# Performance work log

Hardware: AMD Instinct MI355X
Metric: run time of the kernel (lower is better)

Reference implementation:

```python
import jax, jax.numpy as jnp
import numpy as np
from jax import lax

B, C, O, N, L = 32, 32, 32, 512, 128
K, DIL = 2, 2
PAD = (K - 1) * DIL
EPS = 1e-5


def setup_inputs() -> dict:
    key = jax.random.key(0)
    ks = jax.random.split(key, 14)
    x = jax.random.normal(ks[0], (B, C, N, L), dtype=jnp.float32)
    support0 = jax.random.uniform(ks[1], (N, N), dtype=jnp.float32) / N
    support1 = jax.random.uniform(ks[2], (N, N), dtype=jnp.float32) / N
    filt_w = jax.random.normal(ks[3], (O, C, K), dtype=jnp.float32) * 0.1
    filt_b = jnp.zeros((O,), jnp.float32)
    gate_w = jax.random.normal(ks[4], (O, C, K), dtype=jnp.float32) * 0.1
    gate_b = jnp.zeros((O,), jnp.float32)
    gc_w0 = jax.random.normal(ks[5], (O, O), dtype=jnp.float32) * 0.05  # Linear weight (out,in)
    gc_w1 = jax.random.normal(ks[6], (O, O), dtype=jnp.float32) * 0.05
    gc_b = jnp.zeros((O,), jnp.float32)
    skip_w = jax.random.normal(ks[7], (O, O), dtype=jnp.float32) * 0.05  # 1x1 conv
    skip_b = jnp.zeros((O,), jnp.float32)
    res_w = jax.random.normal(ks[8], (C, O), dtype=jnp.float32) * 0.05   # 1x1 conv
    res_b = jnp.zeros((C,), jnp.float32)
    bn_gamma = jnp.ones((C,), jnp.float32)
    bn_beta = jnp.zeros((C,), jnp.float32)
    return dict(x=x, support0=support0, support1=support1,
                filt_w=filt_w, filt_b=filt_b, gate_w=gate_w, gate_b=gate_b,
                gc_w0=gc_w0, gc_w1=gc_w1, gc_b=gc_b,
                skip_w=skip_w, skip_b=skip_b, res_w=res_w, res_b=res_b,
                bn_gamma=bn_gamma, bn_beta=bn_beta)


def _causal_conv(z, w, b):
    # z: (BN, Cin, L), w: (Cout, Cin, K) -> (BN, Cout, L); left-pad for causality
    y = lax.conv_general_dilated(z, w, window_strides=(1,), padding=[(PAD, 0)],
                                 rhs_dilation=(DIL,),
                                 dimension_numbers=('NCH', 'OIH', 'NCH'))
    return y + b[None, :, None]


def reference(x, support0, support1, filt_w, filt_b, gate_w, gate_b,
              gc_w0, gc_w1, gc_b, skip_w, skip_b, res_w, res_b,
              bn_gamma, bn_beta):
    # x: (B, C, N, L)
    x_flat = x.transpose(0, 2, 1, 3).reshape(B * N, C, L)
    h = jnp.tanh(_causal_conv(x_flat, filt_w, filt_b)) * \
        jax.nn.sigmoid(_causal_conv(x_flat, gate_w, gate_b))  # (B*N, O, L)
    h = h.reshape(B, N, O, L)
    # graph conv fused over all timesteps: supports mix node dim, Linear mixes channel dim
    g0 = jnp.einsum('nm,bmcl->bncl', support0, h)
    g1 = jnp.einsum('nm,bmcl->bncl', support1, h)
    hg = (jnp.einsum('bncl,oc->bnol', g0, gc_w0)
          + jnp.einsum('bncl,oc->bnol', g1, gc_w1)
          + gc_b[None, None, :, None])  # (B, N, O, L)
    skip = jnp.einsum('bncl,oc->bnol', hg, skip_w) + skip_b[None, None, :, None]
    skip = skip.transpose(0, 2, 1, 3)  # (B, O, N, L)
    res = jnp.einsum('bncl,oc->bnol', hg, res_w) + res_b[None, None, :, None]  # (B, N, C, L)
    # BatchNorm1d (training mode: batch statistics over (B*N, L) per channel)
    mean = res.mean(axis=(0, 1, 3))
    var = res.var(axis=(0, 1, 3))
    res_bn = bn_gamma[None, None, :, None] * (res - mean[None, None, :, None]) \
             * lax.rsqrt(var[None, None, :, None] + EPS) + bn_beta[None, None, :, None]
    residual = x + res_bn.transpose(0, 2, 1, 3)  # (B, C, N, L); dropout = identity (eval)
    return residual, skip
```

## Files before the change

kernel.cpp:

```cpp
#include <hip/hip_runtime.h>
#include <cstdint>


typedef unsigned short ushort_t;
typedef unsigned int uint_t;

__device__ __forceinline__ float bf2f(uint_t u) {
  return __uint_as_float(u << 16);
}
__device__ __forceinline__ ushort_t f2bf(float f) {
  uint_t u = __float_as_uint(f);
  u += 0x7fffu + ((u >> 16) & 1u);
  return (ushort_t)(u >> 16);
}

__global__ __launch_bounds__(256) void k0(
    const float* __restrict__ gc_w0, const float* __restrict__ gc_w1,
    const float* __restrict__ gc_b, const float* __restrict__ skip_w,
    const float* __restrict__ skip_b, const float* __restrict__ res_w,
    const float* __restrict__ res_b, float* __restrict__ Wc) {
  const int t = threadIdx.x;
  for (int e = t; e < 4096; e += 256) {
    const int mat = e >> 10, idx = e & 1023, o = idx >> 5, ci = idx & 31;
    const float* left = (mat < 2) ? skip_w : res_w;
    const float* g = (mat & 1) ? gc_w1 : gc_w0;
    float s = 0.f;
    #pragma unroll
    for (int c = 0; c < 32; ++c) s = fmaf(left[o * 32 + c], g[c * 32 + ci], s);
    Wc[mat * 1024 + idx] = s;
  }
  if (t < 32) {
    float s = 0.f, r = 0.f;
    #pragma unroll
    for (int c = 0; c < 32; ++c) {
      s = fmaf(skip_w[t * 32 + c], gc_b[c], s);
      r = fmaf(res_w[t * 32 + c], gc_b[c], r);
    }
    Wc[4096 + t] = s + skip_b[t];
    Wc[4128 + t] = r + res_b[t];
  }
}

__global__ __launch_bounds__(256) void k0b(const float* __restrict__ S0,
                                           const float* __restrict__ S1,
                                           ushort_t* __restrict__ S0b,
                                           ushort_t* __restrict__ S1b) {
  const int i = (blockIdx.x * 256 + threadIdx.x) * 4;
  const float4 a = *(const float4*)(S0 + i);
  const float4 c = *(const float4*)(S1 + i);
  ushort4 pa = make_ushort4(f2bf(a.x), f2bf(a.y), f2bf(a.z), f2bf(a.w));
  ushort4 pc = make_ushort4(f2bf(c.x), f2bf(c.y), f2bf(c.z), f2bf(c.w));
  *(ushort4*)(S0b + i) = pa;
  *(ushort4*)(S1b + i) = pc;
}

__global__ __launch_bounds__(256) void k1a(const float* __restrict__ x,
                                           ushort_t* __restrict__ xT) {
  __shared__ float tile[128 * 65];
  const int nt = blockIdx.x, c = blockIdx.y, b = blockIdx.z;
  const int n0 = nt * 64, t = threadIdx.x;
  const int lq = t & 31, r = t >> 5;
  const float* src = x + (((size_t)(b * 32 + c)) * 512 + n0) * 128;
  for (int nr = 0; nr < 8; ++nr) {
    const int nn = nr * 8 + r;
    const float4 v = *(const float4*)(src + nn * 128 + lq * 4);
    tile[(lq * 4 + 0) * 65 + nn] = v.x;
    tile[(lq * 4 + 1) * 65 + nn] = v.y;
    tile[(lq * 4 + 2) * 65 + nn] = v.z;
    tile[(lq * 4 + 3) * 65 + nn] = v.w;
  }
  __syncthreads();
  const int nn2 = t & 63, lg = t >> 6;
  ushort_t* dst = xT + (size_t)b * 128 * 16384 + (size_t)c * 512 + n0 + nn2;
  for (int i = 0; i < 32; ++i) {
    const int l = lg * 32 + i;
    dst[(size_t)l * 16384] = f2bf(tile[l * 65 + nn2]);
  }
}

__global__ __launch_bounds__(256) void k1(
    const ushort_t* __restrict__ xT, const float* __restrict__ fw,
    const float* __restrict__ fb, const float* __restrict__ gw,
    const float* __restrict__ gb, ushort_t* __restrict__ hA) {
  const int l = blockIdx.x, b = blockIdx.y;
  const int t = threadIdx.x;
  const size_t plane = (size_t)(b * 128 + l) * 16384;
  const size_t planem2 = (size_t)(b * 128 + l - 2) * 16384;
  for (int half = 0; half < 2; ++half) {
    const int n = t + half * 256;
    float x0v[32], xmv[32];
    #pragma unroll
    for (int c = 0; c < 32; ++c) {
      x0v[c] = bf2f(xT[plane + c * 512 + n]);
      xmv[c] = (l >= 2) ? bf2f(xT[planem2 + c * 512 + n]) : 0.f;
    }
    #pragma unroll 4
    for (int o = 0; o < 32; ++o) {
      float f = fb[o], g = gb[o];
      #pragma unroll
      for (int c = 0; c < 32; ++c) {
        const float w0 = fw[(o * 32 + c) * 2], w1 = fw[(o * 32 + c) * 2 + 1];
        f = fmaf(w0, xmv[c], fmaf(w1, x0v[c], f));
        const float u0 = gw[(o * 32 + c) * 2], u1 = gw[(o * 32 + c) * 2 + 1];
        g = fmaf(u0, xmv[c], fmaf(u1, x0v[c], g));
      }
      const float e2f = __expf(2.f * f);
      const float th = 1.f - 2.f / (e2f + 1.f);
      const float sg = 1.f / (1.f + __expf(-g));
      hA[plane + o * 512 + n] = f2bf(th * sg);
    }
  }
}

typedef __attribute__((ext_vector_type(8))) short bf16x8;
typedef __attribute__((ext_vector_type(4))) float f32x4;

__global__ __launch_bounds__(256) void k2(
    const ushort_t* __restrict__ hA, const ushort_t* __restrict__ S0b,
    const ushort_t* __restrict__ S1b, const float* __restrict__ Wc,
    ushort_t* __restrict__ skip_raw, ushort_t* __restrict__ res_raw,
    float* __restrict__ part) {
  __shared__ float sm[4352];
  float* g0_s = sm;
  float* g1_s = sm + 2176;

  const int t = threadIdx.x;
  const int w = (blockIdx.x & 7) * 1024 + (blockIdx.x >> 3);
  const int nt = w & 7, jt = (w >> 3) & 31, b = w >> 8;
  const int n0 = nt * 64, j0 = jt * 128;
  const int og = t >> 6, lane = t & 63;
  const int fr = lane & 15;
  const int kq = lane >> 4;

  f32x4 acc0[2][4], acc1[2][4];
  #pragma unroll
  for (int jg = 0; jg < 2; ++jg)
    #pragma unroll
    for (int ng = 0; ng < 4; ++ng) {
      acc0[jg][ng] = {0.f, 0.f, 0.f, 0.f};
      acc1[jg][ng] = {0.f, 0.f, 0.f, 0.f};
    }

  const ushort_t* Ap = hA + (size_t)b * 4096 * 512 +
                       (size_t)(j0 + og * 32 + fr) * 512 + kq * 8;
  const ushort_t* B0p = S0b + (size_t)(n0 + fr) * 512 + kq * 8;
  const ushort_t* B1p = S1b + (size_t)(n0 + fr) * 512 + kq * 8;

  #pragma unroll 2
  for (int m0 = 0; m0 < 512; m0 += 32) {
    const bf16x8 a0 = *(const bf16x8*)(Ap + m0);
    const bf16x8 a1 = *(const bf16x8*)(Ap + 16 * 512 + m0);
    #pragma unroll
    for (int ng = 0; ng < 4; ++ng) {
      const bf16x8 b0 = *(const bf16x8*)(B0p + ng * 16 * 512 + m0);
      const bf16x8 b1 = *(const bf16x8*)(B1p + ng * 16 * 512 + m0);
      acc0[0][ng] =
          __builtin_amdgcn_mfma_f32_16x16x32_bf16(a0, b0, acc0[0][ng], 0, 0, 0);
      acc0[1][ng] =
          __builtin_amdgcn_mfma_f32_16x16x32_bf16(a1, b0, acc0[1][ng], 0, 0, 0);
      acc1[0][ng] =
          __builtin_amdgcn_mfma_f32_16x16x32_bf16(a0, b1, acc1[0][ng], 0, 0, 0);
      acc1[1][ng] =
          __builtin_amdgcn_mfma_f32_16x16x32_bf16(a1, b1, acc1[1][ng], 0, 0, 0);
    }
  }

  const float* A0s = Wc;
  const float* A1s = Wc + 1024;
  const float* A0r = Wc + 2048;
  const float* A1r = Wc + 3072;
  const float* bsv = Wc + 4096;
  const float* brv = Wc + 4128;
  const int n_i = lane;
  float accs[8], accq[8];
  #pragma unroll
  for (int oi = 0; oi < 8; ++oi) { accs[oi] = 0.f; accq[oi] = 0.f; }

  for (int lg = 0; lg < 4; ++lg) {
    if (og == lg) {
      #pragma unroll
      for (int jg = 0; jg < 2; ++jg)
        #pragma unroll
        for (int ng = 0; ng < 4; ++ng)
          #pragma unroll
          for (int r = 0; r < 4; ++r) {
            const int c = jg * 16 + kq * 4 + r;
            const int nn = ng * 16 + fr;
            g0_s[c * 68 + nn] = acc0[jg][ng][r];
            g1_s[c * 68 + nn] = acc1[jg][ng][r];
          }
    }
    __syncthreads();
    float sk[8], rs[8];
    #pragma unroll
    for (int oi = 0; oi < 8; ++oi) {
      sk[oi] = bsv[og * 8 + oi];
      rs[oi] = brv[og * 8 + oi];
    }
    for (int c = 0; c < 32; ++c) {
      const float v0 = g0_s[c * 68 + n_i];
      const float v1 = g1_s[c * 68 + n_i];
      #pragma unroll
      for (int oi = 0; oi < 8; ++oi) {
        const int o = og * 8 + oi;
        sk[oi] = fmaf(A0s[o * 32 + c], v0, fmaf(A1s[o * 32 + c], v1, sk[oi]));
        rs[oi] = fmaf(A0r[o * 32 + c], v0, fmaf(A1r[o * 32 + c], v1, rs[oi]));
      }
    }
    const int l = jt * 4 + lg;
    const size_t base = ((size_t)((b * 128 + l) * 32)) * 512 + n0 + n_i;
    #pragma unroll
    for (int oi = 0; oi < 8; ++oi) {
      const int o = og * 8 + oi;
      skip_raw[base + (size_t)o * 512] = f2bf(sk[oi]);
      res_raw[base + (size_t)o * 512] = f2bf(rs[oi]);
      accs[oi] += rs[oi];
      accq[oi] = fmaf(rs[oi], rs[oi], accq[oi]);
    }
    __syncthreads();
  }

  const int bidx = (b * 32 + jt) * 8 + nt;
  #pragma unroll
  for (int oi = 0; oi < 8; ++oi) {
    float s = accs[oi], q = accq[oi];
    for (int m = 1; m < 64; m <<= 1) {
      s += __shfl_xor(s, m, 64);
      q += __shfl_xor(q, m, 64);
    }
    if (n_i == 0) {
      part[(size_t)(og * 8 + oi) * 8192 + bidx] = s;
      part[(size_t)(32 + og * 8 + oi) * 8192 + bidx] = q;
    }
  }
}

__global__ __launch_bounds__(256) void k2b(const float* __restrict__ part,
                                           float* __restrict__ Wc) {
  const int row = blockIdx.x;
  const int t = threadIdx.x;
  float s = 0.f;
  for (int i = t; i < 8192; i += 256) s += part[(size_t)row * 8192 + i];
  for (int m = 1; m < 64; m <<= 1) s += __shfl_xor(s, m, 64);
  __shared__ float red[4];
  if ((t & 63) == 0) red[t >> 6] = s;
  __syncthreads();
  if (t == 0) Wc[4160 + row] = red[0] + red[1] + red[2] + red[3];
}

__global__ __launch_bounds__(256) void k3(
    const ushort_t* __restrict__ skip_raw, const ushort_t* __restrict__ res_raw,
    const float* __restrict__ x, const float* __restrict__ Wc,
    const float* __restrict__ gamma, const float* __restrict__ beta,
    float* __restrict__ out) {
  __shared__ float tile[64 * 129];
  const int nt = blockIdx.x, ch = blockIdx.y, z = blockIdx.z;
  const int b = z >> 1, tensor = z & 1;
  const int n0 = nt * 64, t = threadIdx.x;
  const ushort_t* src = tensor ? skip_raw : res_raw;
  const int nn = t & 63, lg = t >> 6;
  const size_t sbase = (size_t)(b * 128) * 16384 + (size_t)ch * 512 + n0 + nn;
  for (int i = 0; i < 32; ++i) {
    const int l = lg * 32 + i;
    tile[nn * 129 + l] = bf2f(src[sbase + (size_t)l * 16384]);
  }
  __syncthreads();
  float scale = 1.f, shift = 0.f;
  if (tensor == 0) {
    const float s = Wc[4160 + ch], q = Wc[4192 + ch];
    const float mean = s * (1.f / 2097152.f);
    const float var = q * (1.f / 2097152.f) - mean * mean;
    scale = gamma[ch] * rsqrtf(var + 1e-5f);
    shift = beta[ch] - mean * scale;
  }
  const int l_ = t & 127, ng = t >> 7;
  float* dst = out + (tensor ? 67108864u : 0u);
  for (int j = 0; j < 32; ++j) {
    const int nq = ng * 32 + j;
    float v = tile[nq * 129 + l_] * scale + shift;
    const size_t idx = ((size_t)(b * 32 + ch) * 512 + n0 + nq) * 128 + l_;
    if (tensor == 0) v += x[idx];
    dst[idx] = v;
  }
}

extern "C" void kernel_launch(void* const* d_in, const int* in_sizes, int n_in,
                              void* d_out, int out_size, void* d_ws,
                              size_t ws_size, hipStream_t stream) {
  const float* x = (const float*)d_in[0];
  const float* S0 = (const float*)d_in[1];
  const float* S1 = (const float*)d_in[2];
  const float* fw = (const float*)d_in[3];
  const float* fb = (const float*)d_in[4];
  const float* gw = (const float*)d_in[5];
  const float* gb = (const float*)d_in[6];
  const float* gc_w0 = (const float*)d_in[7];
  const float* gc_w1 = (const float*)d_in[8];
  const float* gc_b = (const float*)d_in[9];
  const float* skip_w = (const float*)d_in[10];
  const float* skip_b = (const float*)d_in[11];
  const float* res_w = (const float*)d_in[12];
  const float* res_b = (const float*)d_in[13];
  const float* gamma = (const float*)d_in[14];
  const float* beta = (const float*)d_in[15];
  float* out = (float*)d_out;

  char* ws = (char*)d_ws;
  float* Wc = (float*)ws;
  ushort_t* hA = (ushort_t*)(ws + 32768);
  ushort_t* xT = (ushort_t*)(ws + 32768 + 134217728ull);
  ushort_t* res_raw = (ushort_t*)(ws + 32768 + 2ull * 134217728ull);
  float* part = (float*)(ws + 32768 + 3ull * 134217728ull);
  ushort_t* S0b = (ushort_t*)(ws + 32768 + 3ull * 134217728ull + 2097152ull);
  ushort_t* S1b = S0b + 262144;

  k0<<<1, 256, 0, stream>>>(gc_w0, gc_w1, gc_b, skip_w, skip_b, res_w, res_b,
                            Wc);
  k0b<<<256, 256, 0, stream>>>(S0, S1, S0b, S1b);
  k1a<<<dim3(8, 32, 32), 256, 0, stream>>>(x, xT);
  k1<<<dim3(128, 32), 256, 0, stream>>>(xT, fw, fb, gw, gb, hA);
  k2<<<8192, 256, 0, stream>>>(hA, S0b, S1b, Wc, xT , res_raw,
                               part);
  k2b<<<64, 256, 0, stream>>>(part, Wc);
  k3<<<dim3(8, 32, 64), 256, 0, stream>>>(xT , res_raw, x, Wc,
                                          gamma, beta, out);
}
```

Baseline: 2.868 ms.

## Stage k2 GEMM operands through double-buffered LDS with register prefetch

```diff
diff --git a/kernel.cpp b/kernel.cpp
--- a/kernel.cpp
+++ b/kernel.cpp
@@ -120,9 +120,9 @@
     const ushort_t* __restrict__ S1b, const float* __restrict__ Wc,
     ushort_t* __restrict__ skip_raw, ushort_t* __restrict__ res_raw,
     float* __restrict__ part) {
-  __shared__ float sm[4352];
-  float* g0_s = sm;
-  float* g1_s = sm + 2176;
+  __shared__ __align__(16) ushort_t smu[20480];
+  float* g0_s = (float*)smu;
+  float* g1_s = (float*)smu + 2176;
 
   const int t = threadIdx.x;
   const int w = (blockIdx.x & 7) * 1024 + (blockIdx.x >> 3);
@@ -141,19 +141,43 @@
       acc1[jg][ng] = {0.f, 0.f, 0.f, 0.f};
     }
 
-  const ushort_t* Ap = hA + (size_t)b * 4096 * 512 +
-                       (size_t)(j0 + og * 32 + fr) * 512 + kq * 8;
-  const ushort_t* B0p = S0b + (size_t)(n0 + fr) * 512 + kq * 8;
-  const ushort_t* B1p = S1b + (size_t)(n0 + fr) * 512 + kq * 8;
-
-  #pragma unroll 2
-  for (int m0 = 0; m0 < 512; m0 += 32) {
-    const bf16x8 a0 = *(const bf16x8*)(Ap + m0);
-    const bf16x8 a1 = *(const bf16x8*)(Ap + 16 * 512 + m0);
+  const int wrow = t >> 2;
+  const int wkc = (t & 3) * 8;
+  const ushort_t* Ag0 = hA + (size_t)b * 4096 * 512 +
+                        (size_t)(j0 + wrow) * 512 + wkc;
+  const ushort_t* Ag1 = Ag0 + (size_t)64 * 512;
+  const ushort_t* Bg0 = S0b + (size_t)(n0 + wrow) * 512 + wkc;
+  const ushort_t* Bg1 = S1b + (size_t)(n0 + wrow) * 512 + wkc;
+  const int wofs = wrow * 40 + wkc;
+
+  uint4 va0 = *(const uint4*)(Ag0);
+  uint4 va1 = *(const uint4*)(Ag1);
+  uint4 vb0 = *(const uint4*)(Bg0);
+  uint4 vb1 = *(const uint4*)(Bg1);
+  *(uint4*)(smu + wofs) = va0;
+  *(uint4*)(smu + 64 * 40 + wofs) = va1;
+  *(uint4*)(smu + 10240 + wofs) = vb0;
+  *(uint4*)(smu + 15360 + wofs) = vb1;
+  __syncthreads();
+
+  int p = 0;
+  for (int ks = 0; ks < 16; ++ks) {
+    if (ks < 15) {
+      const int m0 = (ks + 1) * 32;
+      va0 = *(const uint4*)(Ag0 + m0);
+      va1 = *(const uint4*)(Ag1 + m0);
+      vb0 = *(const uint4*)(Bg0 + m0);
+      vb1 = *(const uint4*)(Bg1 + m0);
+    }
+    const ushort_t* Ab = smu + p * 5120;
+    const ushort_t* Bb0 = smu + 10240 + p * 2560;
+    const ushort_t* Bb1 = smu + 15360 + p * 2560;
+    const bf16x8 a0 = *(const bf16x8*)(Ab + (og * 32 + fr) * 40 + kq * 8);
+    const bf16x8 a1 = *(const bf16x8*)(Ab + (og * 32 + 16 + fr) * 40 + kq * 8);
     #pragma unroll
     for (int ng = 0; ng < 4; ++ng) {
-      const bf16x8 b0 = *(const bf16x8*)(B0p + ng * 16 * 512 + m0);
-      const bf16x8 b1 = *(const bf16x8*)(B1p + ng * 16 * 512 + m0);
+      const bf16x8 b0 = *(const bf16x8*)(Bb0 + (ng * 16 + fr) * 40 + kq * 8);
+      const bf16x8 b1 = *(const bf16x8*)(Bb1 + (ng * 16 + fr) * 40 + kq * 8);
       acc0[0][ng] =
           __builtin_amdgcn_mfma_f32_16x16x32_bf16(a0, b0, acc0[0][ng], 0, 0, 0);
       acc0[1][ng] =
@@ -163,7 +187,17 @@
       acc1[1][ng] =
           __builtin_amdgcn_mfma_f32_16x16x32_bf16(a1, b1, acc1[1][ng], 0, 0, 0);
     }
-  }
+    if (ks < 15) {
+      const int q = p ^ 1;
+      *(uint4*)(smu + q * 5120 + wofs) = va0;
+      *(uint4*)(smu + q * 5120 + 64 * 40 + wofs) = va1;
+      *(uint4*)(smu + 10240 + q * 2560 + wofs) = vb0;
+      *(uint4*)(smu + 15360 + q * 2560 + wofs) = vb1;
+      __syncthreads();
+      p = q;
+    }
+  }
+  __syncthreads();
 
   const float* A0s = Wc;
   const float* A1s = Wc + 1024;
```

Result: faster. 2.497 ms (-12.9%).
